# Kernel tuning notes

Measured on AMD Instinct MI355X. Metric: run time of the kernel, lower is better.

## Reference

```python
import jax, jax.numpy as jnp
import numpy as np
import math

EPS = 1e-5

def setnorm(x, w, b):
    # normalize over (samples, features) per batch element, then per-feature scale/shift
    m = jnp.mean(x, axis=(1, 2), keepdims=True)
    s = jnp.sqrt(jnp.mean(jnp.square(x - m), axis=(1, 2), keepdims=True) + EPS)
    return (x - m) / s * w + b

def setup_inputs() -> dict:
    key = jax.random.key(0)
    ks = jax.random.split(key, 8)
    B, Nx, Ny, dX, dY = 4, 2048, 2048, 256, 256
    sX, sY = 1.0 / math.sqrt(dX), 1.0 / math.sqrt(dY)
    return {
        'X': jax.random.normal(ks[0], (B, Nx, dX), jnp.float32),
        'Y': jax.random.normal(ks[1], (B, Ny, dY), jnp.float32),
        'Wq': jax.random.normal(ks[2], (dY, dX), jnp.float32) * sX,
        'bq': jnp.zeros((dY,), jnp.float32),
        'Wk': jax.random.normal(ks[3], (dY, dY), jnp.float32) * sY,
        'bk': jnp.zeros((dY,), jnp.float32),
        'Wv': jax.random.normal(ks[4], (dY, dY), jnp.float32) * sY,
        'bv': jnp.zeros((dY,), jnp.float32),
        'Wo': jax.random.normal(ks[5], (dX, dY), jnp.float32) * sY,
        'bo': jnp.zeros((dX,), jnp.float32),
        'Wres': jax.random.normal(ks[6], (dX, dX), jnp.float32) * sX,
        'bres': jnp.zeros((dX,), jnp.float32),
        'nq_w': jnp.ones((dX,), jnp.float32), 'nq_b': jnp.zeros((dX,), jnp.float32),
        'nk_w': jnp.ones((dY,), jnp.float32), 'nk_b': jnp.zeros((dY,), jnp.float32),
        'n0_w': jnp.ones((dX,), jnp.float32), 'n0_b': jnp.zeros((dX,), jnp.float32),
    }

def reference(X, Y, Wq, bq, Wk, bk, Wv, bv, Wo, bo, Wres, bres,
              nq_w, nq_b, nk_w, nk_b, n0_w, n0_b):
    num_heads = 8
    dim_Y = Wq.shape[0]
    d = dim_Y // num_heads
    B, Nx, _ = X.shape
    Ny = Y.shape[1]

    Q = setnorm(X, nq_w, nq_b) @ Wq.T + bq          # [B, Nx, dY]
    K = setnorm(Y, nk_w, nk_b) @ Wk.T + bk          # [B, Ny, dY]
    V = Y @ Wv.T + bv                               # [B, Ny, dY]

    # split into heads along feature dim (matches torch split/cat over dim 0)
    Qh = Q.reshape(B, Nx, num_heads, d)
    Kh = K.reshape(B, Ny, num_heads, d)
    Vh = V.reshape(B, Ny, num_heads, d)

    # NOTE: original scales by sqrt(dim_Y), not sqrt(head_dim)
    scores = jnp.einsum('bqhd,bkhd->bhqk', Qh, Kh) / math.sqrt(dim_Y)
    A = jax.nn.softmax(scores, axis=-1)             # [B, H, Nx, Ny]
    Oh = jnp.einsum('bhqk,bkhd->bqhd', A, Vh)       # [B, Nx, H, d]
    O = Oh.reshape(B, Nx, dim_Y) @ Wo.T + bo        # [B, Nx, dX]

    H = X + O
    H = H + jax.nn.relu(setnorm(H, n0_w, n0_b)) @ Wres.T + bres
    return H
```

## Files before the change

kernel.cpp:

```cpp
#include <hip/hip_runtime.h>


typedef _Float16 f16;
typedef _Float16 f16x4 __attribute__((ext_vector_type(4)));
typedef _Float16 f16x8 __attribute__((ext_vector_type(8)));
typedef float f32x4 __attribute__((ext_vector_type(4)));
typedef float f32x16 __attribute__((ext_vector_type(16)));
typedef unsigned int u32;
typedef unsigned int u32x2 __attribute__((ext_vector_type(2)));
typedef unsigned int u32x4 __attribute__((ext_vector_type(4)));

#define DEV static __device__ __forceinline__

DEV void load_lds16(const void* g, void* s) {
  __builtin_amdgcn_global_load_lds(
      (const __attribute__((address_space(1))) void*)g,
      (__attribute__((address_space(3))) void*)s, 16, 0, 0);
}

DEV float fexp2(float x) {
  float r;
  asm("v_exp_f32 %0, %1" : "=v"(r) : "v"(x));
  return r;
}

DEV u32 pkh(float a, float b) {
  auto h = __builtin_amdgcn_cvt_pkrtz(a, b);
  return __builtin_bit_cast(u32, h);
}

__global__ __launch_bounds__(256) void stats_cast(const float* __restrict__ X,
                                                  const float* __restrict__ Y,
                                                  float2* __restrict__ partial,
                                                  const float* __restrict__ w0p, const float* __restrict__ w1p,
                                                  const float* __restrict__ w2p, const float* __restrict__ w3p,
                                                  const float* __restrict__ w4p, f16* __restrict__ wout) {
  const int bid = blockIdx.x;
  if (bid >= 512) {
    const int i8 = (bid - 512) * 256 + threadIdx.x;
    const int mat = i8 >> 13;
    const size_t off = (size_t)(i8 & 8191) * 8;
    const float* src = mat == 0 ? w0p : mat == 1 ? w1p : mat == 2 ? w2p : mat == 3 ? w3p : w4p;
    f32x4 v0 = *reinterpret_cast<const f32x4*>(src + off);
    f32x4 v1 = *reinterpret_cast<const f32x4*>(src + off + 4);
    f16x8 o;
#pragma unroll
    for (int j = 0; j < 4; ++j) { o[j] = (f16)v0[j]; o[j + 4] = (f16)v1[j]; }
    *reinterpret_cast<f16x8*>(wout + (size_t)mat * 65536 + off) = o;
    return;
  }
  const int s = bid >> 6, blk = bid & 63;
  const float* p = (s >= 4 ? Y + (size_t)(s - 4) * 524288 : X + (size_t)s * 524288)
                   + (size_t)blk * 8192;
  float sum = 0.f, ss = 0.f;
#pragma unroll
  for (int j = 0; j < 8; ++j) {
    f32x4 v = *reinterpret_cast<const f32x4*>(p + (size_t)(j * 256 + threadIdx.x) * 4);
#pragma unroll
    for (int e = 0; e < 4; ++e) { sum += v[e]; ss += v[e] * v[e]; }
  }
#pragma unroll
  for (int m = 1; m < 64; m <<= 1) { sum += __shfl_xor(sum, m); ss += __shfl_xor(ss, m); }
  __shared__ float2 red[4];
  if ((threadIdx.x & 63) == 0) red[threadIdx.x >> 6] = make_float2(sum, ss);
  __syncthreads();
  if (threadIdx.x == 0) {
    float a = 0.f, b = 0.f;
    for (int i = 0; i < 4; ++i) { a += red[i].x; b += red[i].y; }
    partial[s * 64 + blk] = make_float2(a, b);
  }
}

DEV float2 finalize_stats(const float2* __restrict__ partial, int s) {
  const int lane = threadIdx.x & 63;
  float2 v = partial[s * 64 + lane];
  float sum = v.x, ss = v.y;
#pragma unroll
  for (int m = 1; m < 64; m <<= 1) { sum += __shfl_xor(sum, m); ss += __shfl_xor(ss, m); }
  const float invN = 1.f / 524288.f;
  const float mean = sum * invN;
  const float var = fmaxf(ss * invN - mean * mean, 0.f);
  return make_float2(mean, rsqrtf(var + 1e-5f));
}

DEV float2 finalize_stats128(const float2* __restrict__ partial, int s) {
  const int lane = threadIdx.x & 63;
  float2 a = partial[s * 128 + lane];
  float2 b = partial[s * 128 + 64 + lane];
  float sum = a.x + b.x, ss = a.y + b.y;
#pragma unroll
  for (int m = 1; m < 64; m <<= 1) { sum += __shfl_xor(sum, m); ss += __shfl_xor(ss, m); }
  const float invN = 1.f / 524288.f;
  const float mean = sum * invN;
  const float var = fmaxf(ss * invN - mean * mean, 0.f);
  return make_float2(mean, rsqrtf(var + 1e-5f));
}

__global__ __launch_bounds__(256) void prep_xy(const float* __restrict__ X,
                                               const float* __restrict__ Y,
                                               f16* __restrict__ Xn, f16* __restrict__ Yn,
                                               f16* __restrict__ Yc,
                                               const float2* __restrict__ partial,
                                               const float* __restrict__ nqw, const float* __restrict__ nqb,
                                               const float* __restrict__ nkw, const float* __restrict__ nkb) {
  const int bid = blockIdx.x;
  const bool isX = bid < 1024;
  const size_t idx = ((size_t)(isX ? bid : bid - 1024) * 256 + threadIdx.x) * 8;
  const int slice = (int)(idx >> 19);
  const float2 st = finalize_stats(partial, (isX ? 0 : 4) + slice);
  const int f = (int)(idx & 255);
  const float* in = isX ? X : Y;
  f32x4 v0 = *reinterpret_cast<const f32x4*>(in + idx);
  f32x4 v1 = *reinterpret_cast<const f32x4*>(in + idx + 4);
  const float* wv = isX ? nqw : nkw;
  const float* bv = isX ? nqb : nkb;
  f32x4 w0 = *reinterpret_cast<const f32x4*>(wv + f);
  f32x4 w1 = *reinterpret_cast<const f32x4*>(wv + f + 4);
  f32x4 b0 = *reinterpret_cast<const f32x4*>(bv + f);
  f32x4 b1 = *reinterpret_cast<const f32x4*>(bv + f + 4);
  f16x8 on;
#pragma unroll
  for (int j = 0; j < 4; ++j) {
    on[j]     = (f16)((v0[j] - st.x) * st.y * w0[j] + b0[j]);
    on[j + 4] = (f16)((v1[j] - st.x) * st.y * w1[j] + b1[j]);
  }
  if (isX) {
    *reinterpret_cast<f16x8*>(Xn + idx) = on;
  } else {
    *reinterpret_cast<f16x8*>(Yn + idx) = on;
    f16x8 oc;
#pragma unroll
    for (int j = 0; j < 4; ++j) { oc[j] = (f16)v0[j]; oc[j + 4] = (f16)v1[j]; }
    *reinterpret_cast<f16x8*>(Yc + idx) = oc;
  }
}

__global__ __launch_bounds__(256) void prep_h(const float* __restrict__ H, f16* __restrict__ out,
                                              const float2* __restrict__ partial2,
                                              const float* __restrict__ w, const float* __restrict__ b) {
  const size_t idx = ((size_t)blockIdx.x * 256 + threadIdx.x) * 8;
  const float2 st = finalize_stats128(partial2, (int)(idx >> 19));
  const int f = (int)(idx & 255);
  f32x4 v0 = *reinterpret_cast<const f32x4*>(H + idx);
  f32x4 v1 = *reinterpret_cast<const f32x4*>(H + idx + 4);
  f32x4 w0 = *reinterpret_cast<const f32x4*>(w + f);
  f32x4 w1 = *reinterpret_cast<const f32x4*>(w + f + 4);
  f32x4 b0 = *reinterpret_cast<const f32x4*>(b + f);
  f32x4 b1 = *reinterpret_cast<const f32x4*>(b + f + 4);
  f16x8 o;
#pragma unroll
  for (int j = 0; j < 4; ++j) {
    o[j]     = (f16)fmaxf((v0[j] - st.x) * st.y * w0[j] + b0[j], 0.f);
    o[j + 4] = (f16)fmaxf((v1[j] - st.x) * st.y * w1[j] + b1[j], 0.f);
  }
  *reinterpret_cast<f16x8*>(out + idx) = o;
}

enum { GM_F16 = 0, GM_VT = 1, GM_F32R = 2 };

template <bool QKV, bool STATS>
__global__ __launch_bounds__(256) void gemm_nt(const f16* __restrict__ A0, const f16* __restrict__ A1,
                                               const f16* __restrict__ A2, const f16* __restrict__ Wc,
                                               const float* __restrict__ b0, const float* __restrict__ b1,
                                               const float* __restrict__ b2,
                                               const float* __restrict__ resid,
                                               void* o0p, void* o1p, void* o2p,
                                               float scale0, int mode0,
                                               float2* __restrict__ spart) {
  __shared__ __align__(16) f16 lds[2][8192];
  __shared__ float2 sred[4];
  const int t = threadIdx.x;
  const int w = t >> 6, lane = t & 63;
  const int g = lane >> 4, lq = lane & 15;
  const int m0 = blockIdx.x * 64, n0 = blockIdx.y * 64;
  const int wr = (w >> 1) * 32, wc = (w & 1) * 32;
  const int z = QKV ? blockIdx.z : 0;

  const f16* A = QKV ? (z == 0 ? A0 : z == 1 ? A1 : A2) : A0;
  const f16* W = QKV ? (Wc + z * 65536) : Wc;
  const float* bias = QKV ? (z == 0 ? b0 : z == 1 ? b1 : b2) : b0;
  void* outp = QKV ? (z == 0 ? o0p : z == 1 ? o1p : o2p) : o0p;
  const float scale = (QKV && z != 0) ? 1.f : scale0;
  const int mode = QKV ? (z == 2 ? GM_VT : GM_F16) : mode0;

  const int r_ = t >> 2, c0 = t & 3, sw = (t >> 3) & 3;
  const int kgA = (c0 ^ sw) << 3;
  const f16* gA = A + (size_t)(m0 + r_) * 256 + kgA;
  const f16* gB = W + (size_t)(n0 + r_) * 256 + kgA;
  f16* dA0 = &lds[0][0] + t * 8;
  f16* dA1 = &lds[1][0] + t * 8;

  f32x4 acc[2][2] = {};

  auto stage = [&](int kt, int buf) {
    f16* base = buf ? dA1 : dA0;
    const int ko = kt * 64;
    load_lds16(gA + ko, base);
    load_lds16(gA + ko + 32, base + 2048);
    load_lds16(gB + ko, base + 4096);
    load_lds16(gB + ko + 32, base + 6144);
  };

  const int swr = ((lq >> 1) & 3);
  auto compute = [&](int buf) {
    const f16* L = &lds[buf][0];
#pragma unroll
    for (int kk = 0; kk < 2; ++kk) {
      f16x8 af[2], bf[2];
#pragma unroll
      for (int i = 0; i < 2; ++i)
        af[i] = *reinterpret_cast<const f16x8*>(L + kk * 2048 + (wr + i * 16 + lq) * 32 + ((g ^ swr) << 3));
#pragma unroll
      for (int j = 0; j < 2; ++j)
        bf[j] = *reinterpret_cast<const f16x8*>(L + 4096 + kk * 2048 + (wc + j * 16 + lq) * 32 + ((g ^ swr) << 3));
#pragma unroll
      for (int i = 0; i < 2; ++i)
#pragma unroll
        for (int j = 0; j < 2; ++j)
          acc[i][j] = __builtin_amdgcn_mfma_f32_16x16x32_f16(af[i], bf[j], acc[i][j], 0, 0, 0);
    }
  };

  stage(0, 0);
  __syncthreads();
  stage(1, 1); compute(0); __syncthreads();
  stage(2, 0); compute(1); __syncthreads();
  stage(3, 1); compute(0); __syncthreads();
  compute(1);

  float tsum = 0.f, tss = 0.f;
#pragma unroll
  for (int i = 0; i < 2; ++i)
#pragma unroll
    for (int j = 0; j < 2; ++j) {
      const int row0 = m0 + wr + i * 16 + g * 4;
      const int col = n0 + wc + j * 16 + lq;
      const float bv = bias[col];
#pragma unroll
      for (int r = 0; r < 4; ++r) {
        const int rr = row0 + r;
        float v = (acc[i][j][r] + bv) * scale;
        if (mode == GM_F16) {
          ((f16*)outp)[(size_t)rr * 256 + col] = (f16)v;
        } else if (mode == GM_VT) {
          ((f16*)outp)[((size_t)(rr >> 11) * 256 + col) * 2048 + (rr & 2047)] = (f16)v;
        } else {
          const size_t o = (size_t)rr * 256 + col;
          const float hval = v + resid[o];
          ((float*)outp)[o] = hval;
          if (STATS) { tsum += hval; tss += hval * hval; }
        }
      }
    }

  if (STATS) {
#pragma unroll
    for (int m = 1; m < 64; m <<= 1) { tsum += __shfl_xor(tsum, m); tss += __shfl_xor(tss, m); }
    __syncthreads();
    if (lane == 0) sred[w] = make_float2(tsum, tss);
    __syncthreads();
    if (t == 0) {
      float a = 0.f, c = 0.f;
      for (int i = 0; i < 4; ++i) { a += sred[i].x; c += sred[i].y; }
      spart[blockIdx.x * 4 + blockIdx.y] = make_float2(a, c);
    }
  }
}

__global__ __launch_bounds__(256, 4) void attn_kernel(const f16* __restrict__ Q,
                                                      const f16* __restrict__ K,
                                                      const f16* __restrict__ Vt,
                                                      f16* __restrict__ O) {
  __shared__ __align__(16) f16 kbuf[2][2][2048];
  __shared__ __align__(16) f16 vbuf[2][2][2048];
  const int t = threadIdx.x;
  const int w = t >> 6, lane = t & 63;
  const int l31 = lane & 31, hi = lane >> 5;
  const int qsub = w & 1, khalf = w >> 1;
  const int wg = blockIdx.x;
  const int linear = (wg & 7) * 128 + (wg >> 3);
  const int qt = linear & 31;
  const int hb = linear >> 5;
  const int h = hb & 7, b = hb >> 3;
  const int q0 = qt * 64 + qsub * 32;

  const f16* Kb = K + (size_t)b * 2048 * 256 + h * 32;
  const f16* Vb = Vt + ((size_t)b * 256 + h * 32) * 2048;

  const f16* qp = Q + (size_t)(b * 2048 + q0 + l31) * 256 + h * 32 + hi * 8;
  const f16x8 qf0 = *reinterpret_cast<const f16x8*>(qp);
  const f16x8 qf1 = *reinterpret_cast<const f16x8*>(qp + 16);

  const f16* gK = Kb + (size_t)(t >> 2) * 256 + (((t & 3) ^ ((t >> 2) & 3)) << 3);
  const f16* gV = Vb + (size_t)(t >> 3) * 2048 + (((t & 7) ^ ((t >> 3) & 7)) << 3);
  const int KSTEP = 64 * 256;
  const int KH = 16 * KSTEP;
  const int VH = 16 * 64;

  const int kR = l31 * 32, kx = l31 & 3;
  const int vR = l31 * 64, vx = l31 & 7;

  f32x16 acc = {};
  float l_ = 0.f;
  const f32x16 zz = {};

  auto stage = [&](int buf) {
    f16* kd = buf ? &kbuf[1][0][0] : &kbuf[0][0][0];
    f16* vd = buf ? &vbuf[1][0][0] : &vbuf[0][0][0];
    load_lds16(gK,      kd + t * 8);
    load_lds16(gK + KH, kd + 2048 + t * 8);
    load_lds16(gV,      vd + t * 8);
    load_lds16(gV + VH, vd + 2048 + t * 8);
    gK += KSTEP; gV += 64;
  };

  auto compute = [&](int buf) {
    const f16* kb = (buf ? &kbuf[1][0][0] : &kbuf[0][0][0]) + khalf * 2048;
    const f16* vb = (buf ? &vbuf[1][0][0] : &vbuf[0][0][0]) + khalf * 2048;
    f16x8 vf[4];
#pragma unroll
    for (int kc = 0; kc < 4; ++kc)
      vf[kc] = *reinterpret_cast<const f16x8*>(vb + vR + ((((kc << 1) | hi) ^ vx) << 3));

#pragma unroll
    for (int kh = 0; kh < 2; ++kh) {
      f16x8 kf0 = *reinterpret_cast<const f16x8*>(kb + kh * 1024 + kR + ((hi ^ kx) << 3));
      f16x8 kf1 = *reinterpret_cast<const f16x8*>(kb + kh * 1024 + kR + (((2 | hi) ^ kx) << 3));
      __builtin_amdgcn_s_setprio(1);
      f32x16 s = __builtin_amdgcn_mfma_f32_32x32x16_f16(kf0, qf0, zz, 0, 0, 0);
      s = __builtin_amdgcn_mfma_f32_32x32x16_f16(kf1, qf1, s, 0, 0, 0);
      __builtin_amdgcn_s_setprio(0);

      float e[16];
#pragma unroll
      for (int i = 0; i < 16; ++i) e[i] = fexp2(s[i]);
      float sa = ((e[0] + e[1]) + (e[2] + e[3])) + ((e[4] + e[5]) + (e[6] + e[7]));
      float sb = ((e[8] + e[9]) + (e[10] + e[11])) + ((e[12] + e[13]) + (e[14] + e[15]));
      l_ += sa + sb;

      u32 pk0 = pkh(e[0], e[1]),   pk1 = pkh(e[2], e[3]);
      u32 pk2 = pkh(e[4], e[5]),   pk3 = pkh(e[6], e[7]);
      u32 pk4 = pkh(e[8], e[9]),   pk5 = pkh(e[10], e[11]);
      u32 pk6 = pkh(e[12], e[13]), pk7 = pkh(e[14], e[15]);

      u32 a0 = pk0, b0 = pk2;
      asm("v_permlane32_swap_b32 %0, %1" : "+v"(a0), "+v"(b0));
      u32 a1 = pk1, b1 = pk3;
      asm("v_permlane32_swap_b32 %0, %1" : "+v"(a1), "+v"(b1));
      u32 c0 = pk4, d0 = pk6;
      asm("v_permlane32_swap_b32 %0, %1" : "+v"(c0), "+v"(d0));
      u32 c1 = pk5, d1 = pk7;
      asm("v_permlane32_swap_b32 %0, %1" : "+v"(c1), "+v"(d1));
      u32x4 paAw = {a0, a1, b0, b1};
      u32x4 paBw = {c0, c1, d0, d1};
      f16x8 paA = __builtin_bit_cast(f16x8, paAw);
      f16x8 paB = __builtin_bit_cast(f16x8, paBw);

      __builtin_amdgcn_s_setprio(1);
      acc = __builtin_amdgcn_mfma_f32_32x32x16_f16(paA, vf[kh * 2 + 0], acc, 0, 0, 0);
      acc = __builtin_amdgcn_mfma_f32_32x32x16_f16(paB, vf[kh * 2 + 1], acc, 0, 0, 0);
      __builtin_amdgcn_s_setprio(0);
    }
  };

  stage(0);
  __syncthreads();

  for (int st = 0; st < 16; st += 2) {
    stage(1);
    compute(0);
    __syncthreads();
    if (st < 14) stage(0);
    compute(1);
    __syncthreads();
  }

  float* cb = reinterpret_cast<float*>(&kbuf[0][0][0]);
  const int slot = (qsub * 64 + lane) * 17;
  if (khalf == 1) {
#pragma unroll
    for (int i = 0; i < 16; ++i) cb[slot + i] = acc[i];
    cb[slot + 16] = l_;
  }
  __syncthreads();
  if (khalf == 0) {
#pragma unroll
    for (int i = 0; i < 16; ++i) acc[i] += cb[slot + i];
    l_ += cb[slot + 16];
    float lf = l_ + __shfl_xor(l_, 32);
    const float inv = 1.f / lf;
#pragma unroll
    for (int i = 0; i < 16; ++i) {
      const int ql = (i & 3) + ((i >> 2) << 3) + (hi << 2);
      const float invq = __shfl(inv, ql);
      const size_t row = (size_t)b * 2048 + q0 + ql;
      O[row * 256 + h * 32 + l31] = (f16)(acc[i] * invq);
    }
  }
}

extern "C" void kernel_launch(void* const* d_in, const int* in_sizes, int n_in,
                              void* d_out, int out_size, void* d_ws, size_t ws_size,
                              hipStream_t stream) {
  (void)in_sizes; (void)n_in; (void)out_size; (void)ws_size;
  const float* X    = (const float*)d_in[0];
  const float* Y    = (const float*)d_in[1];
  const float* Wq   = (const float*)d_in[2];
  const float* bq   = (const float*)d_in[3];
  const float* Wk   = (const float*)d_in[4];
  const float* bk   = (const float*)d_in[5];
  const float* Wv   = (const float*)d_in[6];
  const float* bv   = (const float*)d_in[7];
  const float* Wo   = (const float*)d_in[8];
  const float* bo   = (const float*)d_in[9];
  const float* Wres = (const float*)d_in[10];
  const float* bres = (const float*)d_in[11];
  const float* nq_w = (const float*)d_in[12];
  const float* nq_b = (const float*)d_in[13];
  const float* nk_w = (const float*)d_in[14];
  const float* nk_b = (const float*)d_in[15];
  const float* n0_w = (const float*)d_in[16];
  const float* n0_b = (const float*)d_in[17];
  float* out = (float*)d_out;

  char* ws = (char*)d_ws;
  const size_t MB = 1u << 20;
  f16* bufXn = (f16*)(ws + 0 * MB);
  f16* bufYn = (f16*)(ws + 4 * MB);
  f16* bufYc = (f16*)(ws + 8 * MB);
  f16* bufQ  = (f16*)(ws + 12 * MB);
  f16* bufK  = (f16*)(ws + 16 * MB);
  f16* bufVt = (f16*)(ws + 20 * MB);
  f16* bufW  = (f16*)(ws + 24 * MB);
  float2* partial  = (float2*)(ws + 24 * MB + 700 * 1024);
  float2* partial2 = (float2*)(ws + 24 * MB + 700 * 1024 + 8192);

  stats_cast<<<672, 256, 0, stream>>>(X, Y, partial, Wq, Wk, Wv, Wo, Wres, bufW);

  prep_xy<<<2048, 256, 0, stream>>>(X, Y, bufXn, bufYn, bufYc, partial,
                                    nq_w, nq_b, nk_w, nk_b);

  const float qscale = 1.4426950408889634f / 16.f;
  gemm_nt<true, false><<<dim3(128, 4, 3), 256, 0, stream>>>(
      bufXn, bufYn, bufYc, bufW, bq, bk, bv, nullptr,
      bufQ, bufK, bufVt, qscale, GM_F16, nullptr);

  attn_kernel<<<1024, 256, 0, stream>>>(bufQ, bufK, bufVt, bufXn);

  gemm_nt<false, true><<<dim3(128, 4), 256, 0, stream>>>(
      bufXn, nullptr, nullptr, bufW + 3 * 65536, bo, nullptr, nullptr, X,
      out, nullptr, nullptr, 1.f, GM_F32R, partial2);

  prep_h<<<1024, 256, 0, stream>>>(out, bufYc, partial2, n0_w, n0_b);

  gemm_nt<false, false><<<dim3(128, 4), 256, 0, stream>>>(
      bufYc, nullptr, nullptr, bufW + 4 * 65536, bres, nullptr, nullptr, out,
      out, nullptr, nullptr, 1.f, GM_F32R, nullptr);
}
```

Before: 86.41 us.

## Triple-buffer K/V tiles in attention with vmcnt-based waits

Moves the attention kernel's K/V LDS staging from double to triple buffering. Two tiles are prefetched ahead, and each iteration waits only for the oldest outstanding loads via s_waitcnt vmcnt(4), with one barrier per step instead of two. The goal is to hide more global-load latency. In exchange, LDS use rises from 32KB to 48KB per block and the launch bound drops from 4 to 3 blocks per CU, which lowers occupancy.

New measurement: 91.91 us. 6.4% more time.

```diff
diff --git a/kernel.cpp b/kernel.cpp
--- a/kernel.cpp
+++ b/kernel.cpp
@@ -267,12 +267,12 @@
   }
 }
 
-__global__ __launch_bounds__(256, 4) void attn_kernel(const f16* __restrict__ Q,
+__global__ __launch_bounds__(256, 3) void attn_kernel(const f16* __restrict__ Q,
                                                       const f16* __restrict__ K,
                                                       const f16* __restrict__ Vt,
                                                       f16* __restrict__ O) {
-  __shared__ __align__(16) f16 kbuf[2][2][2048];
-  __shared__ __align__(16) f16 vbuf[2][2][2048];
+  __shared__ __align__(16) f16 kbuf[3][2][2048];
+  __shared__ __align__(16) f16 vbuf[3][2][2048];
   const int t = threadIdx.x;
   const int w = t >> 6, lane = t & 63;
   const int l31 = lane & 31, hi = lane >> 5;
@@ -304,9 +304,9 @@
   float l_ = 0.f;
   const f32x16 zz = {};
 
-  auto stage = [&](int buf) {
-    f16* kd = buf ? &kbuf[1][0][0] : &kbuf[0][0][0];
-    f16* vd = buf ? &vbuf[1][0][0] : &vbuf[0][0][0];
+  auto stageb = [&](int b3) {
+    f16* kd = &kbuf[0][0][0] + b3 * 4096;
+    f16* vd = &vbuf[0][0][0] + b3 * 4096;
     load_lds16(gK,      kd + t * 8);
     load_lds16(gK + KH, kd + 2048 + t * 8);
     load_lds16(gV,      vd + t * 8);
@@ -314,9 +314,9 @@
     gK += KSTEP; gV += 64;
   };
 
-  auto compute = [&](int buf) {
-    const f16* kb = (buf ? &kbuf[1][0][0] : &kbuf[0][0][0]) + khalf * 2048;
-    const f16* vb = (buf ? &vbuf[1][0][0] : &vbuf[0][0][0]) + khalf * 2048;
+  auto compute = [&](int b3) {
+    const f16* kb = &kbuf[0][0][0] + b3 * 4096 + khalf * 2048;
+    const f16* vb = &vbuf[0][0][0] + b3 * 4096 + khalf * 2048;
     f16x8 vf[4];
 #pragma unroll
     for (int kc = 0; kc < 4; ++kc)
@@ -363,17 +363,25 @@
     }
   };
 
-  stage(0);
+  stageb(0);
+  stageb(1);
+  int bs = 2, bc = 0;
+  for (int st = 0; st < 14; ++st) {
+    asm volatile("s_waitcnt vmcnt(4) lgkmcnt(0)" ::: "memory");
+    __builtin_amdgcn_s_barrier();
+    __builtin_amdgcn_sched_barrier(0);
+    stageb(bs); bs = (bs == 2) ? 0 : bs + 1;
+    compute(bc); bc = (bc == 2) ? 0 : bc + 1;
+  }
+  asm volatile("s_waitcnt vmcnt(4) lgkmcnt(0)" ::: "memory");
+  __builtin_amdgcn_s_barrier();
+  __builtin_amdgcn_sched_barrier(0);
+  compute(bc); bc = (bc == 2) ? 0 : bc + 1;
+  asm volatile("s_waitcnt vmcnt(0) lgkmcnt(0)" ::: "memory");
+  __builtin_amdgcn_s_barrier();
+  __builtin_amdgcn_sched_barrier(0);
+  compute(bc);
   __syncthreads();
-
-  for (int st = 0; st < 16; st += 2) {
-    stage(1);
-    compute(0);
-    __syncthreads();
-    if (st < 14) stage(0);
-    compute(1);
-    __syncthreads();
-  }
 
   float* cb = reinterpret_cast<float*>(&kbuf[0][0][0]);
   const int slot = (qsub * 64 + lane) * 17;
```

## Give each attention wave private LDS staging and drop block-wide barriers

Applied to the files above, without the earlier changes.

The attention kernel's K/V staging is restructured so each wave loads its own 32-key K and V tiles into a private double-buffered LDS region. Per-wave s_waitcnt vmcnt ordering replaces the per-step __syncthreads, so the four waves no longer wait on each other inside the key loop. The trade-off is that the two waves sharing a key half now fetch the same K/V data separately, doubling global/L2 load traffic for those tiles, and the loop runs twice as many smaller steps.

New measurement: 91.03 us. +5.3%, slower.

```diff
diff --git a/kernel.cpp b/kernel.cpp
--- a/kernel.cpp
+++ b/kernel.cpp
@@ -271,8 +271,7 @@
                                                       const f16* __restrict__ K,
                                                       const f16* __restrict__ Vt,
                                                       f16* __restrict__ O) {
-  __shared__ __align__(16) f16 kbuf[2][2][2048];
-  __shared__ __align__(16) f16 vbuf[2][2][2048];
+  __shared__ __align__(16) f16 lds[4][2][2048];
   const int t = threadIdx.x;
   const int w = t >> 6, lane = t & 63;
   const int l31 = lane & 31, hi = lane >> 5;
@@ -290,92 +289,103 @@
   const f16* qp = Q + (size_t)(b * 2048 + q0 + l31) * 256 + h * 32 + hi * 8;
   const f16x8 qf0 = *reinterpret_cast<const f16x8*>(qp);
   const f16x8 qf1 = *reinterpret_cast<const f16x8*>(qp + 16);
-
-  const f16* gK = Kb + (size_t)(t >> 2) * 256 + (((t & 3) ^ ((t >> 2) & 3)) << 3);
-  const f16* gV = Vb + (size_t)(t >> 3) * 2048 + (((t & 7) ^ ((t >> 3) & 7)) << 3);
-  const int KSTEP = 64 * 256;
-  const int KH = 16 * KSTEP;
-  const int VH = 16 * 64;
-
-  const int kR = l31 * 32, kx = l31 & 3;
-  const int vR = l31 * 64, vx = l31 & 7;
+  asm volatile("s_waitcnt vmcnt(0)" ::: "memory");
+
+  const int s0 = lane, s1 = lane + 64;
+  const int r0 = s0 >> 2, g0 = (s0 & 3) ^ (r0 & 3);
+  const int r1 = s1 >> 2, g1 = (s1 & 3) ^ (r1 & 3);
+  const f16* gK0 = Kb + (size_t)(khalf * 1024 + r0) * 256 + (g0 << 3);
+  const f16* gK1 = Kb + (size_t)(khalf * 1024 + r1) * 256 + (g1 << 3);
+  const f16* gV0 = Vb + (size_t)r0 * 2048 + khalf * 1024 + (g0 << 3);
+  const f16* gV1 = Vb + (size_t)r1 * 2048 + khalf * 1024 + (g1 << 3);
+  const int KSTEP = 32 * 256;
+
+  f16* wbase = &lds[w][0][0];
+  f16* dK0 = wbase + s0 * 8;
+  f16* dK1 = wbase + s1 * 8;
+  f16* dV0 = wbase + 1024 + s0 * 8;
+  f16* dV1 = wbase + 1024 + s1 * 8;
+
+  auto stageb = [&](int buf) {
+    const int off = buf * 2048;
+    load_lds16(gK0, dK0 + off);
+    load_lds16(gK1, dK1 + off);
+    load_lds16(gV0, dV0 + off);
+    load_lds16(gV1, dV1 + off);
+    gK0 += KSTEP; gK1 += KSTEP; gV0 += 32; gV1 += 32;
+  };
+
+  const int kx = l31 & 3;
+  const int kR = l31 * 32;
 
   f32x16 acc = {};
   float l_ = 0.f;
   const f32x16 zz = {};
 
-  auto stage = [&](int buf) {
-    f16* kd = buf ? &kbuf[1][0][0] : &kbuf[0][0][0];
-    f16* vd = buf ? &vbuf[1][0][0] : &vbuf[0][0][0];
-    load_lds16(gK,      kd + t * 8);
-    load_lds16(gK + KH, kd + 2048 + t * 8);
-    load_lds16(gV,      vd + t * 8);
-    load_lds16(gV + VH, vd + 2048 + t * 8);
-    gK += KSTEP; gV += 64;
+  auto computeb = [&](int buf) {
+    const f16* kb = wbase + buf * 2048;
+    const f16* vb = kb + 1024;
+    f16x8 vf0 = *reinterpret_cast<const f16x8*>(vb + kR + ((hi ^ kx) << 3));
+    f16x8 vf1 = *reinterpret_cast<const f16x8*>(vb + kR + (((2 | hi) ^ kx) << 3));
+    f16x8 kf0 = *reinterpret_cast<const f16x8*>(kb + kR + ((hi ^ kx) << 3));
+    f16x8 kf1 = *reinterpret_cast<const f16x8*>(kb + kR + (((2 | hi) ^ kx) << 3));
+
+    __builtin_amdgcn_s_setprio(1);
+    f32x16 s = __builtin_amdgcn_mfma_f32_32x32x16_f16(kf0, qf0, zz, 0, 0, 0);
+    s = __builtin_amdgcn_mfma_f32_32x32x16_f16(kf1, qf1, s, 0, 0, 0);
+    __builtin_amdgcn_s_setprio(0);
+
+    float e[16];
+#pragma unroll
+    for (int i = 0; i < 16; ++i) e[i] = fexp2(s[i]);
+    float sa = ((e[0] + e[1]) + (e[2] + e[3])) + ((e[4] + e[5]) + (e[6] + e[7]));
+    float sb = ((e[8] + e[9]) + (e[10] + e[11])) + ((e[12] + e[13]) + (e[14] + e[15]));
+    l_ += sa + sb;
+
+    u32 pk0 = pkh(e[0], e[1]),   pk1 = pkh(e[2], e[3]);
+    u32 pk2 = pkh(e[4], e[5]),   pk3 = pkh(e[6], e[7]);
+    u32 pk4 = pkh(e[8], e[9]),   pk5 = pkh(e[10], e[11]);
+    u32 pk6 = pkh(e[12], e[13]), pk7 = pkh(e[14], e[15]);
+
+    u32 a0 = pk0, b0 = pk2;
+    asm("v_permlane32_swap_b32 %0, %1" : "+v"(a0), "+v"(b0));
+    u32 a1 = pk1, b1 = pk3;
+    asm("v_permlane32_swap_b32 %0, %1" : "+v"(a1), "+v"(b1));
+    u32 c0 = pk4, d0 = pk6;
+    asm("v_permlane32_swap_b32 %0, %1" : "+v"(c0), "+v"(d0));
+    u32 c1 = pk5, d1 = pk7;
+    asm("v_permlane32_swap_b32 %0, %1" : "+v"(c1), "+v"(d1));
+    u32x4 paAw = {a0, a1, b0, b1};
+    u32x4 paBw = {c0, c1, d0, d1};
+    f16x8 paA = __builtin_bit_cast(f16x8, paAw);
+    f16x8 paB = __builtin_bit_cast(f16x8, paBw);
+
+    __builtin_amdgcn_s_setprio(1);
+    acc = __builtin_amdgcn_mfma_f32_32x32x16_f16(paA, vf0, acc, 0, 0, 0);
+    acc = __builtin_amdgcn_mfma_f32_32x32x16_f16(paB, vf1, acc, 0, 0, 0);
+    __builtin_amdgcn_s_setprio(0);
   };
 
-  auto compute = [&](int buf) {
-    const f16* kb = (buf ? &kbuf[1][0][0] : &kbuf[0][0][0]) + khalf * 2048;
-    const f16* vb = (buf ? &vbuf[1][0][0] : &vbuf[0][0][0]) + khalf * 2048;
-    f16x8 vf[4];
-#pragma unroll
-    for (int kc = 0; kc < 4; ++kc)
-      vf[kc] = *reinterpret_cast<const f16x8*>(vb + vR + ((((kc << 1) | hi) ^ vx) << 3));
-
-#pragma unroll
-    for (int kh = 0; kh < 2; ++kh) {
-      f16x8 kf0 = *reinterpret_cast<const f16x8*>(kb + kh * 1024 + kR + ((hi ^ kx) << 3));
-      f16x8 kf1 = *reinterpret_cast<const f16x8*>(kb + kh * 1024 + kR + (((2 | hi) ^ kx) << 3));
-      __builtin_amdgcn_s_setprio(1);
-      f32x16 s = __builtin_amdgcn_mfma_f32_32x32x16_f16(kf0, qf0, zz, 0, 0, 0);
-      s = __builtin_amdgcn_mfma_f32_32x32x16_f16(kf1, qf1, s, 0, 0, 0);
-      __builtin_amdgcn_s_setprio(0);
-
-      float e[16];
-#pragma unroll
-      for (int i = 0; i < 16; ++i) e[i] = fexp2(s[i]);
-      float sa = ((e[0] + e[1]) + (e[2] + e[3])) + ((e[4] + e[5]) + (e[6] + e[7]));
-      float sb = ((e[8] + e[9]) + (e[10] + e[11])) + ((e[12] + e[13]) + (e[14] + e[15]));
-      l_ += sa + sb;
-
-      u32 pk0 = pkh(e[0], e[1]),   pk1 = pkh(e[2], e[3]);
-      u32 pk2 = pkh(e[4], e[5]),   pk3 = pkh(e[6], e[7]);
-      u32 pk4 = pkh(e[8], e[9]),   pk5 = pkh(e[10], e[11]);
-      u32 pk6 = pkh(e[12], e[13]), pk7 = pkh(e[14], e[15]);
-
-      u32 a0 = pk0, b0 = pk2;
-      asm("v_permlane32_swap_b32 %0, %1" : "+v"(a0), "+v"(b0));
-      u32 a1 = pk1, b1 = pk3;
-      asm("v_permlane32_swap_b32 %0, %1" : "+v"(a1), "+v"(b1));
-      u32 c0 = pk4, d0 = pk6;
-      asm("v_permlane32_swap_b32 %0, %1" : "+v"(c0), "+v"(d0));
-      u32 c1 = pk5, d1 = pk7;
-      asm("v_permlane32_swap_b32 %0, %1" : "+v"(c1), "+v"(d1));
-      u32x4 paAw = {a0, a1, b0, b1};
-      u32x4 paBw = {c0, c1, d0, d1};
-      f16x8 paA = __builtin_bit_cast(f16x8, paAw);
-      f16x8 paB = __builtin_bit_cast(f16x8, paBw);
-
-      __builtin_amdgcn_s_setprio(1);
-      acc = __builtin_amdgcn_mfma_f32_32x32x16_f16(paA, vf[kh * 2 + 0], acc, 0, 0, 0);
-      acc = __builtin_amdgcn_mfma_f32_32x32x16_f16(paB, vf[kh * 2 + 1], acc, 0, 0, 0);
-      __builtin_amdgcn_s_setprio(0);
+  stageb(0);
+  for (int st = 0; st < 31; st += 2) {
+    stageb(1);
+    asm volatile("s_waitcnt vmcnt(4)" ::: "memory");
+    __builtin_amdgcn_sched_barrier(0);
+    computeb(0);
+    __builtin_amdgcn_sched_barrier(0);
+    if (st < 30) {
+      stageb(0);
+      asm volatile("s_waitcnt vmcnt(4)" ::: "memory");
+    } else {
+      asm volatile("s_waitcnt vmcnt(0)" ::: "memory");
     }
-  };
-
-  stage(0);
+    __builtin_amdgcn_sched_barrier(0);
+    computeb(1);
+    __builtin_amdgcn_sched_barrier(0);
+  }
+
   __syncthreads();
-
-  for (int st = 0; st < 16; st += 2) {
-    stage(1);
-    compute(0);
-    __syncthreads();
-    if (st < 14) stage(0);
-    compute(1);
-    __syncthreads();
-  }
-
-  float* cb = reinterpret_cast<float*>(&kbuf[0][0][0]);
+  float* cb = reinterpret_cast<float*>(&lds[0][0][0]);
   const int slot = (qsub * 64 + lane) * 17;
   if (khalf == 1) {
 #pragma unroll
```
